# Performance work log

Hardware: AMD Instinct MI355X
Metric: run time of the kernel (lower is better)

The kernel has to match this reference:

```python
import jax, jax.numpy as jnp
import numpy as np

D_MODEL = 1024
NUM_HEADS = 16
NUM_KV_HEADS = 4
D_K = D_MODEL // NUM_HEADS              # 64
G = NUM_HEADS // NUM_KV_HEADS           # queries per kv head = 4
B, S = 2, 2048


def setup_inputs() -> dict:
    key = jax.random.key(0)
    ks = jax.random.split(key, 11)
    s = 0.02
    return {
        "query": jax.random.normal(ks[0], (B, S, D_MODEL), jnp.float32),
        "key_in": jax.random.normal(ks[1], (B, S, D_MODEL), jnp.float32),
        "value_in": jax.random.normal(ks[2], (B, S, D_MODEL), jnp.float32),
        "Wq": jax.random.normal(ks[3], (D_MODEL, D_MODEL), jnp.float32) * s,
        "bq": jnp.zeros((D_MODEL,), jnp.float32),
        "Wk": jax.random.normal(ks[4], (D_MODEL, NUM_KV_HEADS * D_K), jnp.float32) * s,
        "bk": jnp.zeros((NUM_KV_HEADS * D_K,), jnp.float32),
        "Wv": jax.random.normal(ks[5], (D_MODEL, NUM_KV_HEADS * D_K), jnp.float32) * s,
        "bv": jnp.zeros((NUM_KV_HEADS * D_K,), jnp.float32),
        "Wo": jax.random.normal(ks[6], (D_MODEL, D_MODEL), jnp.float32) * s,
        "bo": jnp.zeros((D_MODEL,), jnp.float32),
    }


def reference(query, key_in, value_in, Wq, bq, Wk, bk, Wv, bv, Wo, bo):
    scale = jnp.sqrt(jnp.asarray(D_K, query.dtype))
    # Projections
    Q = (query @ Wq + bq).reshape(B, S, NUM_HEADS, D_K).transpose(0, 2, 1, 3)        # [B,H,S,dk]
    K = (key_in @ Wk + bk).reshape(B, S, NUM_KV_HEADS, D_K).transpose(0, 2, 1, 3)    # [B,KVH,S,dk]
    V = (value_in @ Wv + bv).reshape(B, S, NUM_KV_HEADS, D_K).transpose(0, 2, 1, 3)  # [B,KVH,S,dk]
    # repeat_interleave over head dim -> group Q heads by KV head instead
    Qg = Q.reshape(B, NUM_KV_HEADS, G, S, D_K)                                       # [B,KVH,G,S,dk]
    scores = jnp.einsum('bkgqd,bksd->bkgqs', Qg, K) / scale                          # [B,KVH,G,S,S]
    attn = jax.nn.softmax(scores, axis=-1)
    ctx = jnp.einsum('bkgqs,bksd->bkgqd', attn, V)                                   # [B,KVH,G,S,dk]
    ctx = ctx.reshape(B, NUM_HEADS, S, D_K).transpose(0, 2, 1, 3).reshape(B, S, D_MODEL)
    output = ctx @ Wo + bo
    # new_cache: K[:, ::G] on the repeated tensor == original K/V per kv head
    return output, K, V
```

## Files before the change

### kernel.cpp

```cpp
#include <hip/hip_runtime.h>

typedef unsigned short u16;
typedef unsigned int u32;
typedef __attribute__((ext_vector_type(8))) short short8;
typedef __attribute__((ext_vector_type(4))) float f32x4;

#define MFMA16(a, b, c) __builtin_amdgcn_mfma_f32_16x16x32_bf16(a, b, c, 0, 0, 0)

#define SEQ 2048
#define DM 1024

__device__ __forceinline__ u16 f2bf(float f) {
  u32 u = __float_as_uint(f);
  u += 0x7fffu + ((u >> 16) & 1u);
  return (u16)(u >> 16);
}
__device__ __forceinline__ u32 pack2(float a, float b) {
  return (u32)f2bf(a) | ((u32)f2bf(b) << 16);
}
__device__ __forceinline__ u32 pack2t(float a, float b) {
  return __builtin_amdgcn_perm(__float_as_uint(b), __float_as_uint(a), 0x07060302u);
}

template <bool F32>
__device__ __forceinline__ uint4 ld8(const void* p, size_t elem) {
  if constexpr (F32) {
    const float* f = (const float*)p + elem;
    float4 a = *(const float4*)f;
    float4 b = *(const float4*)(f + 4);
    uint4 r;
    r.x = pack2(a.x, a.y);
    r.y = pack2(a.z, a.w);
    r.z = pack2(b.x, b.y);
    r.w = pack2(b.z, b.w);
    return r;
  } else {
    return *(const uint4*)((const u16*)p + elem);
  }
}

__global__ void k_tr(const float* __restrict__ Wq, const float* __restrict__ Wk,
                     const float* __restrict__ Wv, const float* __restrict__ Wo,
                     u16* __restrict__ WqT, u16* __restrict__ WkT, u16* __restrict__ WvT,
                     u16* __restrict__ WoT) {
  const int z = blockIdx.z;
  const float* W = z == 0 ? Wq : (z == 1 ? Wk : (z == 2 ? Wv : Wo));
  u16* Wt = z == 0 ? WqT : (z == 1 ? WkT : (z == 2 ? WvT : WoT));
  const int N = (z == 1 || z == 2) ? 256 : 1024;
  const int n0 = blockIdx.x * 32;
  if (n0 >= N) return;
  const int k0 = blockIdx.y * 32;
  __shared__ float tile[32][33];
  int x = threadIdx.x & 31, y = threadIdx.x >> 5;
#pragma unroll
  for (int i = 0; i < 4; i++)
    tile[y + i * 8][x] = W[(size_t)(k0 + y + i * 8) * N + n0 + x];
  __syncthreads();
#pragma unroll
  for (int i = 0; i < 4; i++)
    Wt[(size_t)(n0 + y + i * 8) * 1024 + k0 + x] = f2bf(tile[x][y + i * 8]);
}

template <bool A32, bool B32>
__device__ __forceinline__ void gemm64(const void* __restrict__ A, const void* __restrict__ Bt,
                                       int m0, int n0, u16* lA, u16* lB, f32x4 acc[2][4]) {
  const int tid = threadIdx.x;
  const int lane = tid & 63, wave = tid >> 6;
  const int l15 = lane & 15, quad = lane >> 4;
  const int wm = wave >> 1, wn = wave & 1;
  const int sr = tid >> 3, scol = (tid & 7) * 8;
  f32x4 zero = {0.f, 0.f, 0.f, 0.f};
#pragma unroll
  for (int i = 0; i < 2; i++)
#pragma unroll
    for (int j = 0; j < 4; j++) acc[i][j] = zero;

  for (int k0 = 0; k0 < 1024; k0 += 64) {
#pragma unroll
    for (int it = 0; it < 2; it++) {
      int r = sr + it * 32;
      *(uint4*)&lA[r * 72 + scol] = ld8<A32>(A, (size_t)(m0 + r) * 1024 + k0 + scol);
    }
#pragma unroll
    for (int it = 0; it < 4; it++) {
      int r = sr + it * 32;
      *(uint4*)&lB[r * 72 + scol] = ld8<B32>(Bt, (size_t)(n0 + r) * 1024 + k0 + scol);
    }
    __syncthreads();
    short8 af[2][2], bfr[4][2];
#pragma unroll
    for (int i = 0; i < 2; i++)
#pragma unroll
      for (int kb = 0; kb < 2; kb++)
        af[i][kb] = *(const short8*)&lA[(wm * 32 + i * 16 + l15) * 72 + kb * 32 + quad * 8];
#pragma unroll
    for (int j = 0; j < 4; j++)
#pragma unroll
      for (int kb = 0; kb < 2; kb++)
        bfr[j][kb] = *(const short8*)&lB[(wn * 64 + j * 16 + l15) * 72 + kb * 32 + quad * 8];
#pragma unroll
    for (int i = 0; i < 2; i++)
#pragma unroll
      for (int j = 0; j < 4; j++) {
        acc[i][j] = MFMA16(af[i][0], bfr[j][0], acc[i][j]);
        acc[i][j] = MFMA16(af[i][1], bfr[j][1], acc[i][j]);
      }
    __syncthreads();
  }
}

__global__ __launch_bounds__(256) void k_proj(
    const float* __restrict__ query, const float* __restrict__ key_in,
    const float* __restrict__ value_in, const u16* __restrict__ WqT,
    const u16* __restrict__ WkT, const u16* __restrict__ WvT, const float* __restrict__ bq,
    const float* __restrict__ bk, const float* __restrict__ bv, u16* __restrict__ qbf,
    float* __restrict__ outK, u16* __restrict__ kbf, float* __restrict__ outV,
    u16* __restrict__ vtb, float qscale) {
  __shared__ u16 lA[64 * 72];
  __shared__ u16 lB[128 * 72];
  const int idx = blockIdx.x;
  const int lane = threadIdx.x & 63, wave = threadIdx.x >> 6;
  const int l15 = lane & 15, quad = lane >> 4;
  const int wm = wave >> 1, wn = wave & 1;
  f32x4 acc[2][4];

  if (idx < 640) {
    const u16* Wt;
    const float* act;
    const float* bias;
    int m0, n0, mode;
    if (idx < 512) {
      Wt = WqT; act = query; bias = bq; m0 = (idx >> 5) * 64; n0 = (idx & 31) * 128; mode = 0;
    } else {
      int i2 = idx - 512;
      Wt = WkT; act = key_in; bias = bk; m0 = (i2 >> 5) * 64; n0 = (i2 & 31) * 128; mode = 1;
    }
    gemm64<false, true>(Wt, act, m0, n0, lA, lB, acc);
#pragma unroll
    for (int i = 0; i < 2; i++) {
      int c0 = m0 + wm * 32 + i * 16 + quad * 4;
      float4 bb = *(const float4*)(bias + c0);
#pragma unroll
      for (int j = 0; j < 4; j++) {
        int token = n0 + wn * 64 + j * 16 + l15;
        int b = token >> 11, s = token & 2047;
        float v0 = acc[i][j][0] + bb.x, v1 = acc[i][j][1] + bb.y;
        float v2 = acc[i][j][2] + bb.z, v3 = acc[i][j][3] + bb.w;
        int d = c0 & 63;
        if (mode == 0) {
          int h = c0 >> 6;
          uint2 o;
          o.x = pack2(v0 * qscale, v1 * qscale);
          o.y = pack2(v2 * qscale, v3 * qscale);
          *(uint2*)(qbf + (((size_t)(b * 16 + h) * SEQ + s) << 6) + d) = o;
        } else {
          int kvh = c0 >> 6;
          size_t ix = (((size_t)(b * 4 + kvh) * SEQ + s) << 6) + d;
          float4 vv = {v0, v1, v2, v3};
          *(float4*)(outK + ix) = vv;
          uint2 o;
          o.x = pack2(v0, v1);
          o.y = pack2(v2, v3);
          *(uint2*)(kbf + ix) = o;
        }
      }
    }
  } else {
    int i2 = idx - 640;
    int m0 = (i2 >> 1) * 64, n0 = (i2 & 1) * 128;
    gemm64<true, false>(value_in, WvT, m0, n0, lA, lB, acc);
#pragma unroll
    for (int i = 0; i < 2; i++) {
      int r0 = m0 + wm * 32 + i * 16 + quad * 4;
      int b = r0 >> 11, s0 = r0 & 2047;
#pragma unroll
      for (int j = 0; j < 4; j++) {
        int col = n0 + wn * 64 + j * 16 + l15;
        int kvh = col >> 6, d = col & 63;
        float bv_ = bv[col];
        float v0 = acc[i][j][0] + bv_, v1 = acc[i][j][1] + bv_;
        float v2 = acc[i][j][2] + bv_, v3 = acc[i][j][3] + bv_;
        size_t base = (((size_t)(b * 4 + kvh) * SEQ + s0) << 6) + d;
        outV[base] = v0;
        outV[base + 64] = v1;
        outV[base + 128] = v2;
        outV[base + 192] = v3;
        uint2 o;
        o.x = pack2(v0, v1);
        o.y = pack2(v2, v3);
        *(uint2*)(vtb + ((size_t)(b * 4 + kvh) * 64 + d) * SEQ + s0) = o;
      }
    }
  }
}

__global__ __launch_bounds__(256) void k_out(const u16* __restrict__ ctxb,
                                             const u16* __restrict__ WoT,
                                             const float* __restrict__ bo,
                                             float* __restrict__ out) {
  __shared__ u16 lA[64 * 72];
  __shared__ u16 lB[128 * 72];
  const int idx = blockIdx.x;
  const int m0 = (idx >> 5) * 64, n0 = (idx & 31) * 128;
  const int lane = threadIdx.x & 63, wave = threadIdx.x >> 6;
  const int l15 = lane & 15, quad = lane >> 4;
  const int wm = wave >> 1, wn = wave & 1;
  f32x4 acc[2][4];
  gemm64<false, false>(WoT, ctxb, m0, n0, lA, lB, acc);
#pragma unroll
  for (int i = 0; i < 2; i++) {
    int c0 = m0 + wm * 32 + i * 16 + quad * 4;
    float4 bb = *(const float4*)(bo + c0);
#pragma unroll
    for (int j = 0; j < 4; j++) {
      int token = n0 + wn * 64 + j * 16 + l15;
      float4 vv = {acc[i][j][0] + bb.x, acc[i][j][1] + bb.y, acc[i][j][2] + bb.z,
                   acc[i][j][3] + bb.w};
      *(float4*)(out + (size_t)token * DM + c0) = vv;
    }
  }
}

__global__ __launch_bounds__(256, 4) void k_flash(const u16* __restrict__ Qh,
                                                  const u16* __restrict__ Kb,
                                                  const u16* __restrict__ Vt,
                                                  u16* __restrict__ ctx) {
  __shared__ u16 lK[128 * 64];
  __shared__ u16 lV[64 * 128];
  __shared__ u16 lP[4 * 16 * 64];
  const int tid = threadIdx.x;
  const int lane = tid & 63, wave = tid >> 6;
  const int l15 = lane & 15, quad = lane >> 4;
  const int bh = blockIdx.y;
  const int b = bh >> 4, h = bh & 15, kvh = h >> 2;
  const u16* Q = Qh + (size_t)bh * SEQ * 64;
  const u16* Kp = Kb + (size_t)(b * 4 + kvh) * SEQ * 64;
  const u16* Vp = Vt + (size_t)(b * 4 + kvh) * 64 * SEQ;
  const int q0 = blockIdx.x * 64 + wave * 16;

  short8 qf[2];
#pragma unroll
  for (int kb = 0; kb < 2; kb++)
    qf[kb] = *(const short8*)(Q + (size_t)(q0 + l15) * 64 + kb * 32 + quad * 8);

  short8 ones8;
  {
    short ov = (l15 == 0) ? (short)0x3F80 : (short)0;
    ones8 = (short8){ov, ov, ov, ov, ov, ov, ov, ov};
  }

  f32x4 zero = {0.f, 0.f, 0.f, 0.f};
  f32x4 acc[4];
  f32x4 lacc = zero;
#pragma unroll
  for (int n = 0; n < 4; n++) acc[n] = zero;

  u16* lPw = lP + wave * (16 * 64);
  const int t8 = tid * 8;

  for (int kc = 0; kc < SEQ; kc += 128) {
    __syncthreads();
#pragma unroll
    for (int i = 0; i < 4; i++) {
      int e = i * 2048 + t8;
      int row = e >> 6, ch = tid & 7;
      uint4 v = *(const uint4*)(Kp + (size_t)kc * 64 + e);
      *(uint4*)&lK[row * 64 + ((ch ^ (row & 7)) << 3)] = v;
    }
#pragma unroll
    for (int i = 0; i < 4; i++) {
      int e = i * 2048 + t8;
      int row = e >> 7, ch = tid & 15;
      uint4 v = *(const uint4*)(Vp + (size_t)row * SEQ + kc + ch * 8);
      *(uint4*)&lV[row * 128 + ((ch ^ (row & 15)) << 3)] = v;
    }
    __syncthreads();

#pragma unroll
    for (int sub = 0; sub < 2; sub++) {
      const int ks = sub * 64;
      f32x4 sc[4];
#pragma unroll
      for (int mt = 0; mt < 4; mt++) {
        int row = ks + mt * 16 + l15;
        short8 kf0 = *(const short8*)&lK[row * 64 + ((quad ^ (row & 7)) << 3)];
        short8 kf1 = *(const short8*)&lK[row * 64 + (((4 + quad) ^ (row & 7)) << 3)];
        f32x4 t = MFMA16(kf0, qf[0], zero);
        sc[mt] = MFMA16(kf1, qf[1], t);
      }
#pragma unroll
      for (int mt = 0; mt < 4; mt++) {
        float e0 = __builtin_amdgcn_exp2f(sc[mt][0]);
        float e1 = __builtin_amdgcn_exp2f(sc[mt][1]);
        float e2 = __builtin_amdgcn_exp2f(sc[mt][2]);
        float e3 = __builtin_amdgcn_exp2f(sc[mt][3]);
        int chp = mt * 2 + (quad >> 1);
        uint2 p;
        p.x = pack2t(e0, e1);
        p.y = pack2t(e2, e3);
        *(uint2*)&lPw[l15 * 64 + ((chp ^ (l15 & 7)) << 3) + (quad & 1) * 4] = p;
      }
      __asm__ volatile("s_waitcnt lgkmcnt(0)" ::: "memory");
#pragma unroll
      for (int kbp = 0; kbp < 2; kbp++) {
        int chq = kbp * 4 + quad;
        short8 pf = *(const short8*)&lPw[l15 * 64 + ((chq ^ (l15 & 7)) << 3)];
        lacc = MFMA16(ones8, pf, lacc);
#pragma unroll
        for (int n = 0; n < 4; n++) {
          int row = n * 16 + l15;
          int chv = sub * 8 + kbp * 4 + quad;
          short8 vf = *(const short8*)&lV[row * 128 + ((chv ^ (row & 15)) << 3)];
          acc[n] = MFMA16(vf, pf, acc[n]);
        }
      }
    }
  }

  float lq = __shfl(lacc[0], l15);
  float inv = __builtin_amdgcn_rcpf(lq);
  u16* base = ctx + ((size_t)(b * SEQ + q0 + l15)) * DM + h * 64;
#pragma unroll
  for (int n = 0; n < 4; n++) {
    uint2 o;
    o.x = pack2t(acc[n][0] * inv, acc[n][1] * inv);
    o.y = pack2t(acc[n][2] * inv, acc[n][3] * inv);
    *(uint2*)(base + n * 16 + quad * 4) = o;
  }
}

extern "C" void kernel_launch(void* const* d_in, const int* in_sizes, int n_in,
                              void* d_out, int out_size, void* d_ws, size_t ws_size,
                              hipStream_t stream) {
  const float* query = (const float*)d_in[0];
  const float* key_in = (const float*)d_in[1];
  const float* value_in = (const float*)d_in[2];
  const float* Wq = (const float*)d_in[3];
  const float* bq = (const float*)d_in[4];
  const float* Wk = (const float*)d_in[5];
  const float* bk = (const float*)d_in[6];
  const float* Wv = (const float*)d_in[7];
  const float* bv = (const float*)d_in[8];
  const float* Wo = (const float*)d_in[9];
  const float* bo = (const float*)d_in[10];

  float* out = (float*)d_out;
  float* outK = out + 4194304;
  float* outV = out + 5242880;

  char* ws = (char*)d_ws;
  u16* WqT = (u16*)(ws);
  u16* WkT = (u16*)(ws + 2097152);
  u16* WvT = (u16*)(ws + 2621440);
  u16* WoT = (u16*)(ws + 3145728);
  u16* qbf = (u16*)(ws + 5242880);
  u16* kbf = (u16*)(ws + 13631488);
  u16* vtb = (u16*)(ws + 15728640);
  u16* ctxb = (u16*)(ws + 17825792);

  const float qscale = 0.125f * 1.44269504088896340736f;

  k_tr<<<dim3(32, 32, 4), 256, 0, stream>>>(Wq, Wk, Wv, Wo, WqT, WkT, WvT, WoT);
  k_proj<<<dim3(768), 256, 0, stream>>>(query, key_in, value_in, WqT, WkT, WvT, bq, bk, bv,
                                        qbf, outK, kbf, outV, vtb, qscale);
  k_flash<<<dim3(32, 32), 256, 0, stream>>>(qbf, kbf, vtb, ctxb);
  k_out<<<dim3(512), 256, 0, stream>>>(ctxb, WoT, bo, out);
}
```

Measured before the change: 212.1 us.

## Pre-convert activations to bf16, use 128x128 GEMM tiles with direct global-to-LDS loads

```diff
diff --git a/kernel.cpp b/kernel.cpp
--- a/kernel.cpp
+++ b/kernel.cpp
@@ -22,84 +22,83 @@
   return __builtin_amdgcn_perm(__float_as_uint(b), __float_as_uint(a), 0x07060302u);
 }
 
-template <bool F32>
-__device__ __forceinline__ uint4 ld8(const void* p, size_t elem) {
-  if constexpr (F32) {
-    const float* f = (const float*)p + elem;
-    float4 a = *(const float4*)f;
-    float4 b = *(const float4*)(f + 4);
-    uint4 r;
-    r.x = pack2(a.x, a.y);
-    r.y = pack2(a.z, a.w);
-    r.z = pack2(b.x, b.y);
-    r.w = pack2(b.z, b.w);
-    return r;
+__device__ __forceinline__ void gl_lds(const u16* g, u16* l) {
+  __builtin_amdgcn_global_load_lds(
+      (const __attribute__((address_space(1))) unsigned int*)(g),
+      (__attribute__((address_space(3))) unsigned int*)(l), 16, 0, 0);
+}
+
+__global__ void k_prep(const float* __restrict__ qin, const float* __restrict__ kin,
+                       const float* __restrict__ vin, const float* __restrict__ Wq,
+                       const float* __restrict__ Wk, const float* __restrict__ Wv,
+                       const float* __restrict__ Wo, u16* __restrict__ qo,
+                       u16* __restrict__ ko, u16* __restrict__ vo,
+                       u16* __restrict__ WqkvT, u16* __restrict__ WoT) {
+  const int y = blockIdx.y;
+  if (y < 3) {
+    const float* in = y == 0 ? qin : (y == 1 ? kin : vin);
+    u16* out = y == 0 ? qo : (y == 1 ? ko : vo);
+    const int n = 2 * SEQ * DM;
+    for (int i = (blockIdx.x * 256 + threadIdx.x) * 4; i < n; i += gridDim.x * 256 * 4) {
+      float4 f = *(const float4*)(in + i);
+      uint2 o;
+      o.x = pack2(f.x, f.y);
+      o.y = pack2(f.z, f.w);
+      *(uint2*)(out + i) = o;
+    }
   } else {
-    return *(const uint4*)((const u16*)p + elem);
-  }
-}
-
-__global__ void k_tr(const float* __restrict__ Wq, const float* __restrict__ Wk,
-                     const float* __restrict__ Wv, const float* __restrict__ Wo,
-                     u16* __restrict__ WqT, u16* __restrict__ WkT, u16* __restrict__ WvT,
-                     u16* __restrict__ WoT) {
-  const int z = blockIdx.z;
-  const float* W = z == 0 ? Wq : (z == 1 ? Wk : (z == 2 ? Wv : Wo));
-  u16* Wt = z == 0 ? WqT : (z == 1 ? WkT : (z == 2 ? WvT : WoT));
-  const int N = (z == 1 || z == 2) ? 256 : 1024;
-  const int n0 = blockIdx.x * 32;
-  if (n0 >= N) return;
-  const int k0 = blockIdx.y * 32;
-  __shared__ float tile[32][33];
-  int x = threadIdx.x & 31, y = threadIdx.x >> 5;
-#pragma unroll
-  for (int i = 0; i < 4; i++)
-    tile[y + i * 8][x] = W[(size_t)(k0 + y + i * 8) * N + n0 + x];
-  __syncthreads();
-#pragma unroll
-  for (int i = 0; i < 4; i++)
-    Wt[(size_t)(n0 + y + i * 8) * 1024 + k0 + x] = f2bf(tile[x][y + i * 8]);
-}
-
-template <bool A32, bool B32>
-__device__ __forceinline__ void gemm64(const void* __restrict__ A, const void* __restrict__ Bt,
-                                       int m0, int n0, u16* lA, u16* lB, f32x4 acc[2][4]) {
+    const int z = y - 3;
+    const float* W = z == 0 ? Wq : (z == 1 ? Wk : (z == 2 ? Wv : Wo));
+    u16* Wt = z == 3 ? WoT : (WqkvT + (z == 0 ? 0 : (z == 1 ? 1024 : 1280)) * 1024);
+    const int N = (z == 1 || z == 2) ? 256 : 1024;
+    const int nt = blockIdx.x & 31, kt = blockIdx.x >> 5;
+    const int n0 = nt * 32;
+    if (n0 >= N) return;
+    const int k0 = kt * 32;
+    __shared__ float tile[32][33];
+    int x = threadIdx.x & 31, yy = threadIdx.x >> 5;
+#pragma unroll
+    for (int i = 0; i < 4; i++)
+      tile[yy + i * 8][x] = W[(size_t)(k0 + yy + i * 8) * N + n0 + x];
+    __syncthreads();
+#pragma unroll
+    for (int i = 0; i < 4; i++)
+      Wt[(size_t)(n0 + yy + i * 8) * 1024 + k0 + x] = f2bf(tile[x][yy + i * 8]);
+  }
+}
+
+__device__ __forceinline__ void gemm128(const u16* __restrict__ A, const u16* __restrict__ Bt,
+                                        int m0, int n0, u16* lA, u16* lB, f32x4 acc[4][4]) {
   const int tid = threadIdx.x;
   const int lane = tid & 63, wave = tid >> 6;
   const int l15 = lane & 15, quad = lane >> 4;
   const int wm = wave >> 1, wn = wave & 1;
-  const int sr = tid >> 3, scol = (tid & 7) * 8;
+  const int lrow = lane >> 3, lcol = (lane & 7) * 8;
   f32x4 zero = {0.f, 0.f, 0.f, 0.f};
 #pragma unroll
-  for (int i = 0; i < 2; i++)
+  for (int i = 0; i < 4; i++)
 #pragma unroll
     for (int j = 0; j < 4; j++) acc[i][j] = zero;
 
   for (int k0 = 0; k0 < 1024; k0 += 64) {
 #pragma unroll
-    for (int it = 0; it < 2; it++) {
-      int r = sr + it * 32;
-      *(uint4*)&lA[r * 72 + scol] = ld8<A32>(A, (size_t)(m0 + r) * 1024 + k0 + scol);
-    }
-#pragma unroll
-    for (int it = 0; it < 4; it++) {
-      int r = sr + it * 32;
-      *(uint4*)&lB[r * 72 + scol] = ld8<B32>(Bt, (size_t)(n0 + r) * 1024 + k0 + scol);
-    }
-    __syncthreads();
-    short8 af[2][2], bfr[4][2];
-#pragma unroll
-    for (int i = 0; i < 2; i++)
-#pragma unroll
-      for (int kb = 0; kb < 2; kb++)
-        af[i][kb] = *(const short8*)&lA[(wm * 32 + i * 16 + l15) * 72 + kb * 32 + quad * 8];
-#pragma unroll
-    for (int j = 0; j < 4; j++)
-#pragma unroll
-      for (int kb = 0; kb < 2; kb++)
-        bfr[j][kb] = *(const short8*)&lB[(wn * 64 + j * 16 + l15) * 72 + kb * 32 + quad * 8];
-#pragma unroll
-    for (int i = 0; i < 2; i++)
+    for (int c = 0; c < 4; c++) {
+      int ch = wave * 4 + c;
+      int row = ch * 8 + lrow;
+      gl_lds(A + (size_t)(m0 + row) * 1024 + k0 + lcol, &lA[ch * 512]);
+      gl_lds(Bt + (size_t)(n0 + row) * 1024 + k0 + lcol, &lB[ch * 512]);
+    }
+    __syncthreads();
+    short8 af[4][2], bfr[4][2];
+#pragma unroll
+    for (int i = 0; i < 4; i++)
+#pragma unroll
+      for (int kb = 0; kb < 2; kb++) {
+        af[i][kb] = *(const short8*)&lA[(wm * 64 + i * 16 + l15) * 64 + kb * 32 + quad * 8];
+        bfr[i][kb] = *(const short8*)&lB[(wn * 64 + i * 16 + l15) * 64 + kb * 32 + quad * 8];
+      }
+#pragma unroll
+    for (int i = 0; i < 4; i++)
 #pragma unroll
       for (int j = 0; j < 4; j++) {
         acc[i][j] = MFMA16(af[i][0], bfr[j][0], acc[i][j]);
@@ -110,106 +109,81 @@
 }
 
 __global__ __launch_bounds__(256) void k_proj(
-    const float* __restrict__ query, const float* __restrict__ key_in,
-    const float* __restrict__ value_in, const u16* __restrict__ WqT,
-    const u16* __restrict__ WkT, const u16* __restrict__ WvT, const float* __restrict__ bq,
-    const float* __restrict__ bk, const float* __restrict__ bv, u16* __restrict__ qbf,
-    float* __restrict__ outK, u16* __restrict__ kbf, float* __restrict__ outV,
-    u16* __restrict__ vtb, float qscale) {
-  __shared__ u16 lA[64 * 72];
-  __shared__ u16 lB[128 * 72];
-  const int idx = blockIdx.x;
+    const u16* __restrict__ WqkvT, const u16* __restrict__ qa, const u16* __restrict__ ka,
+    const u16* __restrict__ va, const float* __restrict__ bq, const float* __restrict__ bk,
+    const float* __restrict__ bv, u16* __restrict__ qbf, float* __restrict__ outK,
+    u16* __restrict__ kbf, float* __restrict__ outV, u16* __restrict__ vtb, float qscale) {
+  __shared__ u16 lA[128 * 64];
+  __shared__ u16 lB[128 * 64];
+  const int m0 = blockIdx.x * 128, n0 = blockIdx.y * 128;
+  const int mode = m0 < 1024 ? 0 : (m0 < 1280 ? 1 : 2);
+  const u16* act = mode == 0 ? qa : (mode == 1 ? ka : va);
+  const float* bias = mode == 0 ? bq : (mode == 1 ? bk : bv);
+  const int cbase = mode == 0 ? 0 : (mode == 1 ? 1024 : 1280);
+
+  f32x4 acc[4][4];
+  gemm128(WqkvT, act, m0, n0, lA, lB, acc);
+
   const int lane = threadIdx.x & 63, wave = threadIdx.x >> 6;
   const int l15 = lane & 15, quad = lane >> 4;
   const int wm = wave >> 1, wn = wave & 1;
-  f32x4 acc[2][4];
-
-  if (idx < 640) {
-    const u16* Wt;
-    const float* act;
-    const float* bias;
-    int m0, n0, mode;
-    if (idx < 512) {
-      Wt = WqT; act = query; bias = bq; m0 = (idx >> 5) * 64; n0 = (idx & 31) * 128; mode = 0;
-    } else {
-      int i2 = idx - 512;
-      Wt = WkT; act = key_in; bias = bk; m0 = (i2 >> 5) * 64; n0 = (i2 & 31) * 128; mode = 1;
-    }
-    gemm64<false, true>(Wt, act, m0, n0, lA, lB, acc);
-#pragma unroll
-    for (int i = 0; i < 2; i++) {
-      int c0 = m0 + wm * 32 + i * 16 + quad * 4;
-      float4 bb = *(const float4*)(bias + c0);
-#pragma unroll
-      for (int j = 0; j < 4; j++) {
-        int token = n0 + wn * 64 + j * 16 + l15;
-        int b = token >> 11, s = token & 2047;
-        float v0 = acc[i][j][0] + bb.x, v1 = acc[i][j][1] + bb.y;
-        float v2 = acc[i][j][2] + bb.z, v3 = acc[i][j][3] + bb.w;
-        int d = c0 & 63;
-        if (mode == 0) {
-          int h = c0 >> 6;
-          uint2 o;
-          o.x = pack2(v0 * qscale, v1 * qscale);
-          o.y = pack2(v2 * qscale, v3 * qscale);
-          *(uint2*)(qbf + (((size_t)(b * 16 + h) * SEQ + s) << 6) + d) = o;
-        } else {
-          int kvh = c0 >> 6;
-          size_t ix = (((size_t)(b * 4 + kvh) * SEQ + s) << 6) + d;
-          float4 vv = {v0, v1, v2, v3};
-          *(float4*)(outK + ix) = vv;
-          uint2 o;
-          o.x = pack2(v0, v1);
-          o.y = pack2(v2, v3);
-          *(uint2*)(kbf + ix) = o;
-        }
-      }
-    }
-  } else {
-    int i2 = idx - 640;
-    int m0 = (i2 >> 1) * 64, n0 = (i2 & 1) * 128;
-    gemm64<true, false>(value_in, WvT, m0, n0, lA, lB, acc);
-#pragma unroll
-    for (int i = 0; i < 2; i++) {
-      int r0 = m0 + wm * 32 + i * 16 + quad * 4;
-      int b = r0 >> 11, s0 = r0 & 2047;
-#pragma unroll
-      for (int j = 0; j < 4; j++) {
-        int col = n0 + wn * 64 + j * 16 + l15;
-        int kvh = col >> 6, d = col & 63;
-        float bv_ = bv[col];
-        float v0 = acc[i][j][0] + bv_, v1 = acc[i][j][1] + bv_;
-        float v2 = acc[i][j][2] + bv_, v3 = acc[i][j][3] + bv_;
-        size_t base = (((size_t)(b * 4 + kvh) * SEQ + s0) << 6) + d;
-        outV[base] = v0;
-        outV[base + 64] = v1;
-        outV[base + 128] = v2;
-        outV[base + 192] = v3;
+#pragma unroll
+  for (int i = 0; i < 4; i++) {
+    int c0 = m0 + wm * 64 + i * 16 + quad * 4;
+    int cv = c0 - cbase;
+    float4 bb = *(const float4*)(bias + cv);
+#pragma unroll
+    for (int j = 0; j < 4; j++) {
+      int token = n0 + wn * 64 + j * 16 + l15;
+      int b = token >> 11, s = token & 2047;
+      float v0 = acc[i][j][0] + bb.x, v1 = acc[i][j][1] + bb.y;
+      float v2 = acc[i][j][2] + bb.z, v3 = acc[i][j][3] + bb.w;
+      if (mode == 0) {
+        int h = cv >> 6, d = cv & 63;
+        uint2 o;
+        o.x = pack2(v0 * qscale, v1 * qscale);
+        o.y = pack2(v2 * qscale, v3 * qscale);
+        *(uint2*)(qbf + (((size_t)(b * 16 + h) * SEQ + s) << 6) + d) = o;
+      } else if (mode == 1) {
+        int kvh = cv >> 6, d = cv & 63;
+        size_t ix = (((size_t)(b * 4 + kvh) * SEQ + s) << 6) + d;
+        float4 vv = {v0, v1, v2, v3};
+        *(float4*)(outK + ix) = vv;
         uint2 o;
         o.x = pack2(v0, v1);
         o.y = pack2(v2, v3);
-        *(uint2*)(vtb + ((size_t)(b * 4 + kvh) * 64 + d) * SEQ + s0) = o;
-      }
-    }
-  }
-}
-
-__global__ __launch_bounds__(256) void k_out(const u16* __restrict__ ctxb,
-                                             const u16* __restrict__ WoT,
+        *(uint2*)(kbf + ix) = o;
+      } else {
+        int kvh = cv >> 6, d = cv & 63;
+        size_t ix = (((size_t)(b * 4 + kvh) * SEQ + s) << 6) + d;
+        float4 vv = {v0, v1, v2, v3};
+        *(float4*)(outV + ix) = vv;
+        size_t tb = ((size_t)(b * 4 + kvh) * 64 + d) * SEQ + s;
+        vtb[tb] = f2bf(v0);
+        vtb[tb + SEQ] = f2bf(v1);
+        vtb[tb + 2 * SEQ] = f2bf(v2);
+        vtb[tb + 3 * SEQ] = f2bf(v3);
+      }
+    }
+  }
+}
+
+__global__ __launch_bounds__(256) void k_out(const u16* __restrict__ WoT,
+                                             const u16* __restrict__ ctxb,
                                              const float* __restrict__ bo,
                                              float* __restrict__ out) {
-  __shared__ u16 lA[64 * 72];
-  __shared__ u16 lB[128 * 72];
-  const int idx = blockIdx.x;
-  const int m0 = (idx >> 5) * 64, n0 = (idx & 31) * 128;
+  __shared__ u16 lA[128 * 64];
+  __shared__ u16 lB[128 * 64];
+  const int m0 = blockIdx.x * 128, n0 = blockIdx.y * 128;
+  f32x4 acc[4][4];
+  gemm128(WoT, ctxb, m0, n0, lA, lB, acc);
+
   const int lane = threadIdx.x & 63, wave = threadIdx.x >> 6;
   const int l15 = lane & 15, quad = lane >> 4;
   const int wm = wave >> 1, wn = wave & 1;
-  f32x4 acc[2][4];
-  gemm64<false, false>(WoT, ctxb, m0, n0, lA, lB, acc);
-#pragma unroll
-  for (int i = 0; i < 2; i++) {
-    int c0 = m0 + wm * 32 + i * 16 + quad * 4;
+#pragma unroll
+  for (int i = 0; i < 4; i++) {
+    int c0 = m0 + wm * 64 + i * 16 + quad * 4;
     float4 bb = *(const float4*)(bo + c0);
 #pragma unroll
     for (int j = 0; j < 4; j++) {
@@ -349,20 +323,22 @@
   float* outV = out + 5242880;
 
   char* ws = (char*)d_ws;
-  u16* WqT = (u16*)(ws);
-  u16* WkT = (u16*)(ws + 2097152);
-  u16* WvT = (u16*)(ws + 2621440);
-  u16* WoT = (u16*)(ws + 3145728);
-  u16* qbf = (u16*)(ws + 5242880);
-  u16* kbf = (u16*)(ws + 13631488);
-  u16* vtb = (u16*)(ws + 15728640);
-  u16* ctxb = (u16*)(ws + 17825792);
+  u16* q_act = (u16*)(ws);
+  u16* k_act = (u16*)(ws + 8388608);
+  u16* v_act = (u16*)(ws + 16777216);
+  u16* WqkvT = (u16*)(ws + 25165824);
+  u16* WoT = (u16*)(ws + 28311552);
+  u16* qbf = (u16*)(ws + 30408704);
+  u16* kbf = (u16*)(ws + 38797312);
+  u16* vtb = (u16*)(ws + 40894464);
+  u16* ctxb = (u16*)(ws + 42991616);
 
   const float qscale = 0.125f * 1.44269504088896340736f;
 
-  k_tr<<<dim3(32, 32, 4), 256, 0, stream>>>(Wq, Wk, Wv, Wo, WqT, WkT, WvT, WoT);
-  k_proj<<<dim3(768), 256, 0, stream>>>(query, key_in, value_in, WqT, WkT, WvT, bq, bk, bv,
-                                        qbf, outK, kbf, outV, vtb, qscale);
+  k_prep<<<dim3(1024, 7), 256, 0, stream>>>(query, key_in, value_in, Wq, Wk, Wv, Wo, q_act,
+                                            k_act, v_act, WqkvT, WoT);
+  k_proj<<<dim3(12, 32), 256, 0, stream>>>(WqkvT, q_act, k_act, v_act, bq, bk, bv, qbf,
+                                           outK, kbf, outV, vtb, qscale);
   k_flash<<<dim3(32, 32), 256, 0, stream>>>(qbf, kbf, vtb, ctxb);
-  k_out<<<dim3(512), 256, 0, stream>>>(ctxb, WoT, bo, out);
-}
+  k_out<<<dim3(8, 32), 256, 0, stream>>>(WoT, ctxb, bo, out);
+}
```

Measured after the change: 221.1 us. +4.2%, slower.
